# Kernel optimization log

Hardware: AMD Instinct MI355X
Metric: run time of the kernel (lower is better)

The kernel has to match this reference:

```python
import jax, jax.numpy as jnp
import numpy as np

DIM = 256; HEADS = 8; WS = 7; ALPHA = 0.5
HD = DIM // HEADS                      # head_dim = 32
GH = int(HEADS * ALPHA); LH = HEADS - GH   # 4 global / 4 local heads
GD = GH * HD; LD = LH * HD             # 128 / 128
HID = int(DIM * 4.0)                   # mlp hidden = 1024
SCALE = HD ** -0.5


def ln(x, g, b, eps=1e-5):
    m = jnp.mean(x, -1, keepdims=True)
    v = jnp.var(x, -1, keepdims=True)
    return (x - m) * jax.lax.rsqrt(v + eps) * g + b


def setup_inputs() -> dict:
    key = jax.random.key(0)
    ks = jax.random.split(key, 12)
    B, H, W = 4, 112, 112
    N = H * W
    def p(k, shape, s=0.02):
        return jax.random.normal(k, shape, jnp.float32) * s
    return {
        'x': jax.random.normal(ks[0], (B, N, DIM), jnp.float32),
        'x_reverse': jax.random.normal(ks[1], (B, N, DIM), jnp.float32),
        'g1': jnp.ones((DIM,), jnp.float32), 'b1': jnp.zeros((DIM,), jnp.float32),
        'g2': jnp.ones((DIM,), jnp.float32), 'b2': jnp.zeros((DIM,), jnp.float32),
        'Gq_w': p(ks[2], (DIM, GD)), 'Gq_b': jnp.zeros((GD,), jnp.float32),
        'Gkv_w': p(ks[3], (DIM, 2 * GD)), 'Gkv_b': jnp.zeros((2 * GD,), jnp.float32),
        'Gp_w': p(ks[4], (GD, GD)), 'Gp_b': jnp.zeros((GD,), jnp.float32),
        'Lq_w': p(ks[5], (DIM, LD)), 'Lq_b': jnp.zeros((LD,), jnp.float32),
        'Lkv_w': p(ks[6], (DIM, 2 * LD)), 'Lkv_b': jnp.zeros((2 * LD,), jnp.float32),
        'Lp_w': p(ks[7], (LD, LD)), 'Lp_b': jnp.zeros((LD,), jnp.float32),
        'fc1_w': p(ks[8], (DIM, HID)), 'fc1_b': jnp.zeros((HID,), jnp.float32),
        'dw_w': p(ks[9], (HID, 1, 3, 3), 0.05), 'dw_b': jnp.zeros((HID,), jnp.float32),
        'fc2_w': p(ks[10], (HID, DIM)), 'fc2_b': jnp.zeros((DIM,), jnp.float32),
        'H': 112, 'W': 112,
    }


def reference(x, x_reverse, g1, b1, g2, b2,
              Gq_w, Gq_b, Gkv_w, Gkv_b, Gp_w, Gp_b,
              Lq_w, Lq_b, Lkv_w, Lkv_b, Lp_w, Lp_b,
              fc1_w, fc1_b, dw_w, dw_b, fc2_w, fc2_b, H, W):
    B, N, C = x.shape
    assert H % WS == 0 and W % WS == 0  # shapes chosen so no padding branch
    xn = ln(x, g1, b1).reshape(B, H, W, C)
    xrn = ln(x_reverse, g1, b1).reshape(B, H, W, C)

    # ---- Global attention: queries from every pixel, kv from avg-pooled (ws x ws) grid
    q = (xn.reshape(B, N, C) @ Gq_w + Gq_b).reshape(B, N, GH, HD)
    pooled = xrn.reshape(B, H // WS, WS, W // WS, WS, C).mean(axis=(2, 4)).reshape(B, -1, C)
    kv = (pooled @ Gkv_w + Gkv_b).reshape(B, -1, 2, GH, HD)
    k, v = kv[:, :, 0], kv[:, :, 1]
    a = jax.nn.softmax(jnp.einsum('bnhd,bmhd->bhnm', q, k) * SCALE, axis=-1)
    g_out = jnp.einsum('bhnm,bmhd->bnhd', a, v).reshape(B, H, W, GD) @ Gp_w + Gp_b

    # ---- Local windowed attention (ws x ws non-overlapping windows)
    hg, wg = H // WS, W // WS
    TG, T = hg * wg, WS * WS
    def windows(t):
        return t.reshape(B, hg, WS, wg, WS, C).transpose(0, 1, 3, 2, 4, 5).reshape(B, TG, T, C)
    xw, xrw = windows(xn), windows(xrn)
    ql = (xw @ Lq_w + Lq_b).reshape(B, TG, T, LH, HD)
    kvl = (xrw @ Lkv_w + Lkv_b).reshape(B, TG, T, 2, LH, HD)
    kl, vl = kvl[:, :, :, 0], kvl[:, :, :, 1]
    al = jax.nn.softmax(jnp.einsum('bgqhd,bgkhd->bghqk', ql, kl) * SCALE, axis=-1)
    lo = jnp.einsum('bghqk,bgkhd->bgqhd', al, vl).reshape(B, hg, wg, WS, WS, LD)
    lo = lo.transpose(0, 1, 3, 2, 4, 5).reshape(B, H, W, LD) @ Lp_w + Lp_b

    x = x + jnp.concatenate([g_out, lo], axis=-1).reshape(B, N, C)

    # ---- DWMlp: fc1 -> depthwise 3x3 conv -> GELU -> fc2
    h = ln(x, g2, b2) @ fc1_w + fc1_b
    himg = h.reshape(B, H, W, HID).transpose(0, 3, 1, 2)
    himg = jax.lax.conv_general_dilated(
        himg, dw_w, (1, 1), 'SAME', feature_group_count=HID,
        dimension_numbers=('NCHW', 'OIHW', 'NCHW')) + dw_b[None, :, None, None]
    h = jax.nn.gelu(himg.reshape(B, HID, N).transpose(0, 2, 1), approximate=False)
    return x + (h @ fc2_w + fc2_b)
```

## Files before the change

kernel.cpp:

```cpp
#include <hip/hip_runtime.h>
#include <hip/hip_bf16.h>
#include <math.h>

typedef __hip_bfloat16 bf16;
typedef __attribute__((ext_vector_type(8))) short bf16x8;
typedef __attribute__((ext_vector_type(4))) float f32x4;

static constexpr int B_  = 4;
static constexpr int Hh  = 112, Ww = 112;
static constexpr int Nn  = Hh * Ww;
static constexpr int Cc  = 256;
static constexpr int M_  = B_ * Nn;
static constexpr int GH_ = 4;
static constexpr int GD_ = 128;
static constexpr int LD_ = 128;
static constexpr int HID_ = 1024;
static constexpr int TG_ = 256;
static constexpr int T__ = 49;
static constexpr float SCALE_ = 0.17677669529663687f;

__device__ __forceinline__ float toF(const bf16 v)  { return __bfloat162float(v); }
__device__ __forceinline__ float toF(const float v) { return v; }
__device__ __forceinline__ void st_out(float* p, float v) { *p = v; }
__device__ __forceinline__ void st_out(bf16* p, float v)  { *p = __float2bfloat16(v); }

__device__ __forceinline__ void gload_lds16(const bf16* g, bf16* l) {
  using gvoid = const __attribute__((address_space(1))) void;
  using lvoid = __attribute__((address_space(3))) void;
  __builtin_amdgcn_global_load_lds((gvoid*)g, (lvoid*)l, 16, 0, 0);
}

__device__ __forceinline__ int win_row_map(int r) {
  int b  = r / Nn;
  int rr = r - b * Nn;
  int g  = rr / T__;
  int t  = rr - g * T__;
  int gh = g >> 4, gw = g & 15;
  int i  = t / 7,  j  = t - i * 7;
  int n  = (gh * 7 + i) * Ww + gw * 7 + j;
  return b * Nn + n;
}

__global__ void guard_fill_kernel(float* out) {
  out[threadIdx.x + blockIdx.x * 256] = 1.0e6f;
}

__global__ __launch_bounds__(256) void convert_all_kernel(
    const float* __restrict__ s0, const float* __restrict__ s1,
    const float* __restrict__ s2, const float* __restrict__ s3,
    const float* __restrict__ s4, const float* __restrict__ s5,
    const float* __restrict__ s6, const float* __restrict__ s7,
    bf16* __restrict__ wt) {
  int idx = blockIdx.x * 256 + threadIdx.x;
  const float* W; int K, N, base;
  if      (idx < 32768)  { W = s0; K = 256;  N = 128;  base = 0; }
  else if (idx < 98304)  { W = s1; K = 256;  N = 256;  base = 32768; }
  else if (idx < 114688) { W = s2; K = 128;  N = 128;  base = 98304; }
  else if (idx < 147456) { W = s3; K = 256;  N = 128;  base = 114688; }
  else if (idx < 212992) { W = s4; K = 256;  N = 256;  base = 147456; }
  else if (idx < 229376) { W = s5; K = 128;  N = 128;  base = 212992; }
  else if (idx < 491520) { W = s6; K = 256;  N = 1024; base = 229376; }
  else                   { W = s7; K = 1024; N = 256;  base = 491520; }
  int loc = idx - base;
  int n = loc / K, k = loc - n * K;
  wt[idx] = __float2bfloat16(W[(size_t)k * N + n]);
}

__global__ __launch_bounds__(256) void ln_dual_kernel(const float* __restrict__ x,
                                                      const float* __restrict__ xr,
                                                      const float* __restrict__ g,
                                                      const float* __restrict__ bta,
                                                      bf16* __restrict__ xn,
                                                      bf16* __restrict__ xrn) {
  const int tid = threadIdx.x;
  const int row = blockIdx.x * 4 + (tid >> 6);
  const int lane = tid & 63;
  const int c0 = lane * 4;
  const float* src = blockIdx.y ? xr : x;
  bf16* dst = blockIdx.y ? xrn : xn;
  float4 v = *(const float4*)(src + (size_t)row * Cc + c0);
  float s  = v.x + v.y + v.z + v.w;
  float ss = v.x * v.x + v.y * v.y + v.z * v.z + v.w * v.w;
  #pragma unroll
  for (int off = 1; off < 64; off <<= 1) {
    s  += __shfl_xor(s, off);
    ss += __shfl_xor(ss, off);
  }
  float mean = s * (1.0f / Cc);
  float var  = ss * (1.0f / Cc) - mean * mean;
  float r = rsqrtf(var + 1e-5f);
  float4 gv = *(const float4*)(g + c0);
  float4 bv = *(const float4*)(bta + c0);
  bf16 o[4];
  o[0] = __float2bfloat16((v.x - mean) * r * gv.x + bv.x);
  o[1] = __float2bfloat16((v.y - mean) * r * gv.y + bv.y);
  o[2] = __float2bfloat16((v.z - mean) * r * gv.z + bv.z);
  o[3] = __float2bfloat16((v.w - mean) * r * gv.w + bv.w);
  *(uint2*)(dst + (size_t)row * Cc + c0) = *(uint2*)o;
}

__global__ __launch_bounds__(64) void pool_kernel(const bf16* __restrict__ xrn,
                                                  bf16* __restrict__ pooled) {
  const int lane = threadIdx.x;
  const int c0 = lane * 4;
  const int g  = blockIdx.x;
  const int b  = blockIdx.y;
  const int gh = g >> 4, gw = g & 15;
  float acc[4] = {};
  union U4 { uint2 u; bf16 e[4]; };
  #pragma unroll
  for (int i = 0; i < 7; i++)
    for (int j = 0; j < 7; j++) {
      int n = (gh * 7 + i) * Ww + gw * 7 + j;
      U4 r4;
      r4.u = *(const uint2*)(xrn + ((size_t)b * Nn + n) * Cc + c0);
      #pragma unroll
      for (int u = 0; u < 4; u++) acc[u] += toF(r4.e[u]);
    }
  bf16 o[4];
  #pragma unroll
  for (int u = 0; u < 4; u++) o[u] = __float2bfloat16(acc[u] * (1.0f / 49.0f));
  *(uint2*)(pooled + ((size_t)b * TG_ + g) * Cc + c0) = *(uint2*)o;
}

template <typename OutT, bool WIN_A, bool RES>
__global__ __launch_bounds__(256) void mfma_gemm_kernel(const bf16* __restrict__ A,
                                                        const bf16* __restrict__ Wt,
                                                        const float* __restrict__ bias,
                                                        const float* __restrict__ res,
                                                        OutT* __restrict__ out,
                                                        int M, int N, int K) {
  __shared__ __align__(16) bf16 As[128 * 32];
  __shared__ __align__(16) bf16 Bs[128 * 32];
  const int tid = threadIdx.x;
  const int bm = blockIdx.y * 128, bn = blockIdx.x * 128;
  const int lane = tid & 63, w = tid >> 6;
  const int wm = (w >> 1) * 64, wn = (w & 1) * 64;

  const int srow0 = w * 32 + (lane >> 2);
  const int srow1 = srow0 + 16;
  const int kq    = (lane & 3) * 8;
  const int ar0 = bm + srow0, ar1 = bm + srow1;
  const int as0 = WIN_A ? win_row_map(ar0) : ar0;
  const int as1 = WIN_A ? win_row_map(ar1) : ar1;
  const bf16* Ag0 = A  + (size_t)as0 * K + kq;
  const bf16* Ag1 = A  + (size_t)as1 * K + kq;
  const bf16* Bg0 = Wt + (size_t)(bn + srow0) * K + kq;
  const bf16* Bg1 = Wt + (size_t)(bn + srow1) * K + kq;
  bf16* Al0 = &As[srow0 * 32 + kq];
  bf16* Al1 = &As[srow1 * 32 + kq];
  bf16* Bl0 = &Bs[srow0 * 32 + kq];
  bf16* Bl1 = &Bs[srow1 * 32 + kq];

  f32x4 acc[4][4];
  #pragma unroll
  for (int i = 0; i < 4; i++)
    #pragma unroll
    for (int j = 0; j < 4; j++) acc[i][j] = (f32x4){0.f, 0.f, 0.f, 0.f};

  const int r16  = lane & 15;
  const int koct = (lane >> 4) * 8;
  const int mrow = wm + r16;
  const int nrow = wn + r16;

  for (int k0 = 0; k0 < K; k0 += 32) {
    gload_lds16(Ag0 + k0, Al0);
    gload_lds16(Ag1 + k0, Al1);
    gload_lds16(Bg0 + k0, Bl0);
    gload_lds16(Bg1 + k0, Bl1);
    __syncthreads();
    bf16x8 af[4], bfr[4];
    #pragma unroll
    for (int i = 0; i < 4; i++) af[i]  = *(const bf16x8*)&As[(mrow + i * 16) * 32 + koct];
    #pragma unroll
    for (int j = 0; j < 4; j++) bfr[j] = *(const bf16x8*)&Bs[(nrow + j * 16) * 32 + koct];
    #pragma unroll
    for (int i = 0; i < 4; i++)
      #pragma unroll
      for (int j = 0; j < 4; j++)
        acc[i][j] = __builtin_amdgcn_mfma_f32_16x16x32_bf16(af[i], bfr[j], acc[i][j], 0, 0, 0);
    __syncthreads();
  }

  const int r0 = (lane >> 4) * 4;
  #pragma unroll
  for (int j = 0; j < 4; j++) {
    const int col = bn + wn + j * 16 + r16;
    const float bv = bias[col];
    #pragma unroll
    for (int i = 0; i < 4; i++) {
      const int rowb = bm + wm + i * 16 + r0;
      #pragma unroll
      for (int r = 0; r < 4; r++) {
        size_t ro = (size_t)(rowb + r) * N + col;
        float v = acc[i][j][r] + bv;
        if (RES) v += res[ro];
        st_out(out + ro, v);
      }
    }
  }
}

__global__ __launch_bounds__(256) void gattn_kernel(const bf16* __restrict__ q,
                                                    const bf16* __restrict__ kv,
                                                    bf16* __restrict__ out) {
  __shared__ __align__(16) bf16 Ks[256][40];
  __shared__ __align__(16) bf16 Vt[32][264];
  __shared__ __align__(16) bf16 Ps[4][32][40];
  const int tid = threadIdx.x;
  const int lane = tid & 63, w = tid >> 6;
  const int h = blockIdx.y, b = blockIdx.z;
  const int n0 = blockIdx.x * 128;
  const int r16 = lane & 15, oct = (lane >> 4) * 8;
  const bf16* kvb = kv + (size_t)b * TG_ * 256;

  {
    const int key = tid;
    const bf16* kp = kvb + (size_t)key * 256 + h * 32;
    *(uint4*)&Ks[key][0]  = *(const uint4*)(kp);
    *(uint4*)&Ks[key][8]  = *(const uint4*)(kp + 8);
    *(uint4*)&Ks[key][16] = *(const uint4*)(kp + 16);
    *(uint4*)&Ks[key][24] = *(const uint4*)(kp + 24);
    union { uint4 u[4]; bf16 e[32]; } vv;
    vv.u[0] = *(const uint4*)(kp + 128);
    vv.u[1] = *(const uint4*)(kp + 136);
    vv.u[2] = *(const uint4*)(kp + 144);
    vv.u[3] = *(const uint4*)(kp + 152);
    #pragma unroll
    for (int d = 0; d < 32; d++) Vt[d][key] = vv.e[d];
  }
  const size_t qbase0 = ((size_t)(b * Nn + n0 + w * 32 + r16)) * GD_ + h * 32 + oct;
  bf16x8 aq0 = *(const bf16x8*)(q + qbase0);
  bf16x8 aq1 = *(const bf16x8*)(q + qbase0 + (size_t)16 * GD_);
  __syncthreads();

  f32x4 rs0 = {0.f, 0.f, 0.f, 0.f}, rs1 = {0.f, 0.f, 0.f, 0.f};
  f32x4 ov[2][2];
  #pragma unroll
  for (int i = 0; i < 2; i++)
    #pragma unroll
    for (int dt = 0; dt < 2; dt++) ov[i][dt] = (f32x4){0.f, 0.f, 0.f, 0.f};

  for (int c0 = 0; c0 < 256; c0 += 32) {
    #pragma unroll
    for (int t = 0; t < 2; t++) {
      bf16x8 bk = *(const bf16x8*)&Ks[c0 + t * 16 + r16][oct];
      f32x4 s0 = __builtin_amdgcn_mfma_f32_16x16x32_bf16(aq0, bk, (f32x4){0.f,0.f,0.f,0.f}, 0, 0, 0);
      f32x4 s1 = __builtin_amdgcn_mfma_f32_16x16x32_bf16(aq1, bk, (f32x4){0.f,0.f,0.f,0.f}, 0, 0, 0);
      const int prow = (lane >> 4) * 4;
      const int pcol = t * 16 + r16;
      #pragma unroll
      for (int r = 0; r < 4; r++) {
        bf16 pb0 = __float2bfloat16(__expf(s0[r] * SCALE_));
        bf16 pb1 = __float2bfloat16(__expf(s1[r] * SCALE_));
        rs0[r] += toF(pb0);
        rs1[r] += toF(pb1);
        Ps[w][prow + r][pcol]      = pb0;
        Ps[w][16 + prow + r][pcol] = pb1;
      }
    }
    bf16x8 ap0 = *(const bf16x8*)&Ps[w][r16][oct];
    bf16x8 ap1 = *(const bf16x8*)&Ps[w][16 + r16][oct];
    #pragma unroll
    for (int dt = 0; dt < 2; dt++) {
      bf16x8 bv = *(const bf16x8*)&Vt[dt * 16 + r16][c0 + oct];
      ov[0][dt] = __builtin_amdgcn_mfma_f32_16x16x32_bf16(ap0, bv, ov[0][dt], 0, 0, 0);
      ov[1][dt] = __builtin_amdgcn_mfma_f32_16x16x32_bf16(ap1, bv, ov[1][dt], 0, 0, 0);
    }
  }
  #pragma unroll
  for (int off = 1; off < 16; off <<= 1) {
    #pragma unroll
    for (int r = 0; r < 4; r++) {
      rs0[r] += __shfl_xor(rs0[r], off);
      rs1[r] += __shfl_xor(rs1[r], off);
    }
  }
  const int orow0 = b * Nn + n0 + w * 32 + (lane >> 4) * 4;
  #pragma unroll
  for (int r = 0; r < 4; r++) {
    float inv0 = 1.0f / rs0[r];
    float inv1 = 1.0f / rs1[r];
    size_t ro0 = (size_t)(orow0 + r) * GD_ + h * 32;
    size_t ro1 = ro0 + (size_t)16 * GD_;
    #pragma unroll
    for (int dt = 0; dt < 2; dt++) {
      out[ro0 + dt * 16 + r16] = __float2bfloat16(ov[0][dt][r] * inv0);
      out[ro1 + dt * 16 + r16] = __float2bfloat16(ov[1][dt][r] * inv1);
    }
  }
}

__global__ __launch_bounds__(64) void lattn_kernel(const bf16* __restrict__ ql,
                                                   const bf16* __restrict__ kvl,
                                                   bf16* __restrict__ out) {
  __shared__ float ks[T__ * 32];
  __shared__ float vs[T__ * 32];
  const int tid = threadIdx.x;
  const int h = blockIdx.x, g = blockIdx.y, b = blockIdx.z;
  const size_t base = (((size_t)b * TG_ + g) * T__) * 256;
  for (int idx = tid; idx < T__ * 32; idx += 64) {
    int m = idx >> 5, d = idx & 31;
    ks[idx] = toF(kvl[base + (size_t)m * 256 + h * 32 + d]);
    vs[idx] = toF(kvl[base + (size_t)m * 256 + 128 + h * 32 + d]);
  }
  __syncthreads();
  if (tid < T__) {
    const size_t qoff = (((size_t)b * TG_ + g) * T__ + tid) * LD_ + h * 32;
    float qv[32];
    #pragma unroll
    for (int d = 0; d < 32; d++) qv[d] = toF(ql[qoff + d]) * SCALE_;
    float l = 0.f;
    float acc[32] = {};
    for (int m = 0; m < T__; m++) {
      const float* kr = ks + m * 32;
      const float* vr = vs + m * 32;
      float s = 0.f;
      #pragma unroll
      for (int d = 0; d < 32; d++) s = fmaf(qv[d], kr[d], s);
      float p = __expf(fminf(s, 60.f));
      l += p;
      #pragma unroll
      for (int d = 0; d < 32; d++) acc[d] = fmaf(p, vr[d], acc[d]);
    }
    const float rl = 1.0f / l;
    #pragma unroll
    for (int d = 0; d < 32; d++) out[qoff + d] = __float2bfloat16(acc[d] * rl);
  }
}

__global__ __launch_bounds__(256) void combine_ln_kernel(const float* __restrict__ x,
                                                         const bf16* __restrict__ gout,
                                                         const bf16* __restrict__ lo_w,
                                                         const float* __restrict__ g2,
                                                         const float* __restrict__ b2,
                                                         float* __restrict__ xres,
                                                         bf16* __restrict__ xn2) {
  const int tid = threadIdx.x;
  const int row = blockIdx.x * 4 + (tid >> 6);
  const int lane = tid & 63;
  const int c0 = lane * 4;
  int b = row / Nn, n = row - b * Nn;
  int y = n / Ww, xx = n - y * Ww;
  int gh = y / 7, i = y - gh * 7;
  int gw = xx / 7, j = xx - gw * 7;
  size_t wrow = ((size_t)b * TG_ + gh * 16 + gw) * T__ + i * 7 + j;
  union U4 { uint2 u; bf16 e[4]; } r4;
  if (lane < 32) r4.u = *(const uint2*)(gout + (size_t)row * GD_ + c0);
  else           r4.u = *(const uint2*)(lo_w + wrow * LD_ + (c0 - 128));
  float4 v = *(const float4*)(x + (size_t)row * Cc + c0);
  v.x += toF(r4.e[0]); v.y += toF(r4.e[1]); v.z += toF(r4.e[2]); v.w += toF(r4.e[3]);
  *(float4*)(xres + (size_t)row * Cc + c0) = v;
  float s  = v.x + v.y + v.z + v.w;
  float ss = v.x * v.x + v.y * v.y + v.z * v.z + v.w * v.w;
  #pragma unroll
  for (int off = 1; off < 64; off <<= 1) {
    s  += __shfl_xor(s, off);
    ss += __shfl_xor(ss, off);
  }
  float mean = s * (1.0f / Cc);
  float var  = ss * (1.0f / Cc) - mean * mean;
  float r = rsqrtf(var + 1e-5f);
  float4 gv = *(const float4*)(g2 + c0);
  float4 bv = *(const float4*)(b2 + c0);
  bf16 o[4];
  o[0] = __float2bfloat16((v.x - mean) * r * gv.x + bv.x);
  o[1] = __float2bfloat16((v.y - mean) * r * gv.y + bv.y);
  o[2] = __float2bfloat16((v.z - mean) * r * gv.z + bv.z);
  o[3] = __float2bfloat16((v.w - mean) * r * gv.w + bv.w);
  *(uint2*)(xn2 + (size_t)row * Cc + c0) = *(uint2*)o;
}

static constexpr int TW_ = 14;
__global__ __launch_bounds__(256) void dwconv_gelu_kernel(const bf16* __restrict__ h1,
                                                          const float* __restrict__ w,
                                                          const float* __restrict__ bias,
                                                          bf16* __restrict__ h2) {
  const int tid = threadIdx.x;
  const int c0 = tid * 4;
  const int img = blockIdx.z, y = blockIdx.y;
  const int xt = blockIdx.x * TW_;
  const size_t ibase = (size_t)img * Nn * HID_;

  float wreg[9][4], breg[4];
  #pragma unroll
  for (int u = 0; u < 4; u++) {
    breg[u] = bias[c0 + u];
    #pragma unroll
    for (int t = 0; t < 9; t++) wreg[t][u] = w[(c0 + u) * 9 + t];
  }

  const bf16* rowp[3];
  bool rok[3];
  #pragma unroll
  for (int r = 0; r < 3; r++) {
    int yy = y - 1 + r;
    rok[r] = (yy >= 0 && yy < Hh);
    rowp[r] = h1 + ibase + (size_t)(rok[r] ? yy : 0) * Ww * HID_ + c0;
  }

  float wa[3][4], wb[3][4], wc[3][4];
  union U4 { ushort2 u2[2]; bf16 e[4]; };
  auto loadcol = [&](int xcol, float v[3][4]) {
    if (xcol < 0 || xcol >= Ww) {
      #pragma unroll
      for (int r = 0; r < 3; r++)
        #pragma unroll
        for (int u = 0; u < 4; u++) v[r][u] = 0.f;
      return;
    }
    #pragma unroll
    for (int r = 0; r < 3; r++) {
      if (rok[r]) {
        U4 raw;
        *(uint2*)&raw = *(const uint2*)(rowp[r] + (size_t)xcol * HID_);
        #pragma unroll
        for (int u = 0; u < 4; u++) v[r][u] = toF(raw.e[u]);
      } else {
        #pragma unroll
        for (int u = 0; u < 4; u++) v[r][u] = 0.f;
      }
    }
  };
  loadcol(xt - 1, wa);
  loadcol(xt, wb);

  for (int xx = 0; xx < TW_; xx++) {
    const int x = xt + xx;
    loadcol(x + 1, wc);
    bf16 res[4];
    #pragma unroll
    for (int u = 0; u < 4; u++) {
      float a = breg[u];
      a = fmaf(wa[0][u], wreg[0][u], a);
      a = fmaf(wb[0][u], wreg[1][u], a);
      a = fmaf(wc[0][u], wreg[2][u], a);
      a = fmaf(wa[1][u], wreg[3][u], a);
      a = fmaf(wb[1][u], wreg[4][u], a);
      a = fmaf(wc[1][u], wreg[5][u], a);
      a = fmaf(wa[2][u], wreg[6][u], a);
      a = fmaf(wb[2][u], wreg[7][u], a);
      a = fmaf(wc[2][u], wreg[8][u], a);
      float gl = 0.5f * a * (1.0f + erff(a * 0.7071067811865475f));
      res[u] = __float2bfloat16(gl);
    }
    *(uint2*)(h2 + ibase + (size_t)(y * Ww + x) * HID_ + c0) = *(uint2*)res;
    #pragma unroll
    for (int r = 0; r < 3; r++)
      #pragma unroll
      for (int u = 0; u < 4; u++) { wa[r][u] = wb[r][u]; wb[r][u] = wc[r][u]; }
  }
}

extern "C" void kernel_launch(void* const* d_in, const int* in_sizes, int n_in,
                              void* d_out, int out_size, void* d_ws, size_t ws_size,
                              hipStream_t stream) {
  const float* x     = (const float*)d_in[0];
  const float* xrev  = (const float*)d_in[1];
  const float* g1    = (const float*)d_in[2];
  const float* b1    = (const float*)d_in[3];
  const float* g2    = (const float*)d_in[4];
  const float* b2    = (const float*)d_in[5];
  const float* Gq_w  = (const float*)d_in[6];
  const float* Gq_b  = (const float*)d_in[7];
  const float* Gkv_w = (const float*)d_in[8];
  const float* Gkv_b = (const float*)d_in[9];
  const float* Gp_w  = (const float*)d_in[10];
  const float* Gp_b  = (const float*)d_in[11];
  const float* Lq_w  = (const float*)d_in[12];
  const float* Lq_b  = (const float*)d_in[13];
  const float* Lkv_w = (const float*)d_in[14];
  const float* Lkv_b = (const float*)d_in[15];
  const float* Lp_w  = (const float*)d_in[16];
  const float* Lp_b  = (const float*)d_in[17];
  const float* fc1_w = (const float*)d_in[18];
  const float* fc1_b = (const float*)d_in[19];
  const float* dw_w  = (const float*)d_in[20];
  const float* dw_b  = (const float*)d_in[21];
  const float* fc2_w = (const float*)d_in[22];
  const float* fc2_b = (const float*)d_in[23];

  const size_t E_GQ = 256 * 128, E_GKV = 256 * 256, E_GP = 128 * 128;
  const size_t E_LQ = 256 * 128, E_LKV = 256 * 256, E_LP = 128 * 128;
  const size_t E_F1 = 256 * 1024, E_F2 = 1024 * 256;
  char* ws = (char*)d_ws;
  bf16* Gq_t  = (bf16*)ws;
  bf16* Gkv_t = Gq_t  + E_GQ;
  bf16* Gp_t  = Gkv_t + E_GKV;
  bf16* Lq_t  = Gp_t  + E_GP;
  bf16* Lkv_t = Lq_t  + E_LQ;
  bf16* Lp_t  = Lkv_t + E_LKV;
  bf16* f1_t  = Lp_t  + E_LP;
  bf16* f2_t  = f1_t  + E_F1;
  const size_t WT_ELEMS = E_GQ + E_GKV + E_GP + E_LQ + E_LKV + E_LP + E_F1 + E_F2;
  const size_t WT_BYTES = WT_ELEMS * 2;

  const size_t SZ_ROW2 = (size_t)M_ * Cc * 2;
  const size_t SZ_HALF = (size_t)M_ * 128 * 2;
  const size_t SZ_POOL = (size_t)B_ * TG_ * Cc * 2;
  const size_t SZ_KVG  = (size_t)B_ * TG_ * 256 * 2;
  const size_t SZ_H    = (size_t)(2 * Nn) * HID_ * 2;
  char* arena = ws + WT_BYTES;
  bf16* S1 = (bf16*)(arena);
  bf16* S2 = (bf16*)(arena + SZ_ROW2);
  bf16* S3 = (bf16*)(arena + 2 * SZ_ROW2);
  bf16* S4 = (bf16*)(arena + 2 * SZ_ROW2 + SZ_HALF);
  bf16* S5 = (bf16*)(arena + 2 * SZ_ROW2 + 2 * SZ_HALF);
  bf16* poolb = (bf16*)(arena + 2 * SZ_ROW2 + 3 * SZ_HALF);
  bf16* kvG   = (bf16*)(arena + 2 * SZ_ROW2 + 3 * SZ_HALF + SZ_POOL);
  const size_t ARENA_A = 2 * SZ_ROW2 + 3 * SZ_HALF + SZ_POOL + SZ_KVG;
  bf16* xn2 = S1;
  bf16* h1  = (bf16*)(arena + SZ_ROW2);
  bf16* h2  = (bf16*)(arena + SZ_ROW2 + SZ_H);
  const size_t ARENA_B = SZ_ROW2 + 2 * SZ_H;

  float* out  = (float*)d_out;
  float* xres = (float*)d_out;
  const size_t NEED = WT_BYTES + (ARENA_A > ARENA_B ? ARENA_A : ARENA_B);
  if (ws_size < NEED) {
    guard_fill_kernel<<<16, 256, 0, stream>>>(out);
    return;
  }

  bf16* xn = S1;  bf16* xrn = S2;  bf16* qbuf = S3;  bf16* gattn = S4;  bf16* gout = S5;
  bf16* kvl = S1; bf16* lo_w = S2; bf16* qlb  = S3;  bf16* lattn = S4;

  convert_all_kernel<<<2944, 256, 0, stream>>>(Gq_w, Gkv_w, Gp_w, Lq_w, Lkv_w, Lp_w,
                                               fc1_w, fc2_w, (bf16*)ws);
  ln_dual_kernel<<<dim3(M_ / 4, 2), 256, 0, stream>>>(x, xrev, g1, b1, xn, xrn);
  pool_kernel<<<dim3(TG_, B_), 64, 0, stream>>>(xrn, poolb);
  mfma_gemm_kernel<bf16, false, false><<<dim3(1, M_ / 128), 256, 0, stream>>>(
      xn, Gq_t, Gq_b, nullptr, qbuf, M_, 128, 256);
  mfma_gemm_kernel<bf16, false, false><<<dim3(2, 8), 256, 0, stream>>>(
      poolb, Gkv_t, Gkv_b, nullptr, kvG, 1024, 256, 256);
  gattn_kernel<<<dim3(Nn / 128, GH_, B_), 256, 0, stream>>>(qbuf, kvG, gattn);
  mfma_gemm_kernel<bf16, false, false><<<dim3(1, M_ / 128), 256, 0, stream>>>(
      gattn, Gp_t, Gp_b, nullptr, gout, M_, 128, 128);
  mfma_gemm_kernel<bf16, true, false><<<dim3(1, M_ / 128), 256, 0, stream>>>(
      xn, Lq_t, Lq_b, nullptr, qlb, M_, 128, 256);
  mfma_gemm_kernel<bf16, true, false><<<dim3(2, M_ / 128), 256, 0, stream>>>(
      xrn, Lkv_t, Lkv_b, nullptr, kvl, M_, 256, 256);
  lattn_kernel<<<dim3(4, TG_, B_), 64, 0, stream>>>(qlb, kvl, lattn);
  mfma_gemm_kernel<bf16, false, false><<<dim3(1, M_ / 128), 256, 0, stream>>>(
      lattn, Lp_t, Lp_b, nullptr, lo_w, M_, 128, 128);
  combine_ln_kernel<<<M_ / 4, 256, 0, stream>>>(x, gout, lo_w, g2, b2, xres, xn2);
  for (int half = 0; half < 2; half++) {
    const size_t r0 = (size_t)half * 2 * Nn;
    mfma_gemm_kernel<bf16, false, false><<<dim3(8, (2 * Nn) / 128), 256, 0, stream>>>(
        xn2 + r0 * Cc, f1_t, fc1_b, nullptr, h1, 2 * Nn, 1024, 256);
    dwconv_gelu_kernel<<<dim3(Ww / TW_, Hh, 2), 256, 0, stream>>>(h1, dw_w, dw_b, h2);
    mfma_gemm_kernel<float, false, true><<<dim3(2, (2 * Nn) / 128), 256, 0, stream>>>(
        h2, f2_t, fc2_b, xres + r0 * Cc, out + r0 * Cc, 2 * Nn, 256, 1024);
  }
}
```

Before: 556.2 us.

## Rewrite local window attention with MFMA, one block per window

The local attention kernel changes from one thread per query doing scalar fp32 dot products over shared-memory K/V to a 256-thread block per window, with each wave handling one head. QK^T and PV now use bf16 16x16x32 MFMA instructions. K is staged row-major, V is staged transposed, and the bf16 probabilities are written to shared memory. The 49-token window is padded to 64 with masking and zeroed V columns. This removes the scalar FMA bottleneck and the idle lanes of the old 64-thread blocks. In exchange, P is quantized to bf16, and the score clamp before exp is dropped, so there is no overflow guard.

```diff
diff --git a/kernel.cpp b/kernel.cpp
--- a/kernel.cpp
+++ b/kernel.cpp
@@ -291,41 +291,106 @@
   }
 }
 
-__global__ __launch_bounds__(64) void lattn_kernel(const bf16* __restrict__ ql,
-                                                   const bf16* __restrict__ kvl,
-                                                   bf16* __restrict__ out) {
-  __shared__ float ks[T__ * 32];
-  __shared__ float vs[T__ * 32];
+__global__ __launch_bounds__(256) void lattn_kernel(const bf16* __restrict__ ql,
+                                                    const bf16* __restrict__ kvl,
+                                                    bf16* __restrict__ out) {
+  __shared__ __align__(16) bf16 Ks[4][64][40];
+  __shared__ __align__(16) bf16 Vt[4][32][72];
+  __shared__ __align__(16) bf16 Ps[4][64][72];
   const int tid = threadIdx.x;
-  const int h = blockIdx.x, g = blockIdx.y, b = blockIdx.z;
-  const size_t base = (((size_t)b * TG_ + g) * T__) * 256;
-  for (int idx = tid; idx < T__ * 32; idx += 64) {
-    int m = idx >> 5, d = idx & 31;
-    ks[idx] = toF(kvl[base + (size_t)m * 256 + h * 32 + d]);
-    vs[idx] = toF(kvl[base + (size_t)m * 256 + 128 + h * 32 + d]);
+  const int lane = tid & 63, w = tid >> 6;
+  const int g = blockIdx.x, b = blockIdx.y;
+  const int r16 = lane & 15, oct = (lane >> 4) * 8;
+  const size_t wbase = ((size_t)b * TG_ + g) * T__;
+
+  for (int u = tid; u < T__ * 32; u += 256) {
+    int m = u >> 5, c8 = u & 31;
+    union { uint4 q4; bf16 e[8]; } ch;
+    ch.q4 = *(const uint4*)(kvl + (wbase + m) * 256 + c8 * 8);
+    if (c8 < 16) {
+      int h = c8 >> 2, d0 = (c8 & 3) * 8;
+      *(uint4*)&Ks[h][m][d0] = ch.q4;
+    } else {
+      int cv = c8 - 16;
+      int h = cv >> 2, d0 = (cv & 3) * 8;
+      #pragma unroll
+      for (int e = 0; e < 8; e++) Vt[h][d0 + e][m] = ch.e[e];
+    }
+  }
+  for (int z = tid; z < 4 * 32 * 15; z += 256) {
+    int h = z / 480, rem = z - h * 480;
+    int d = rem / 15, key = 49 + (rem - d * 15);
+    Vt[h][d][key] = __float2bfloat16(0.f);
+  }
+  bf16x8 aq[4];
+  #pragma unroll
+  for (int i = 0; i < 4; i++) {
+    int qr = 16 * i + r16;
+    if (qr > 48) qr = 48;
+    aq[i] = *(const bf16x8*)(ql + (wbase + qr) * LD_ + w * 32 + oct);
   }
   __syncthreads();
-  if (tid < T__) {
-    const size_t qoff = (((size_t)b * TG_ + g) * T__ + tid) * LD_ + h * 32;
-    float qv[32];
-    #pragma unroll
-    for (int d = 0; d < 32; d++) qv[d] = toF(ql[qoff + d]) * SCALE_;
-    float l = 0.f;
-    float acc[32] = {};
-    for (int m = 0; m < T__; m++) {
-      const float* kr = ks + m * 32;
-      const float* vr = vs + m * 32;
-      float s = 0.f;
-      #pragma unroll
-      for (int d = 0; d < 32; d++) s = fmaf(qv[d], kr[d], s);
-      float p = __expf(fminf(s, 60.f));
-      l += p;
-      #pragma unroll
-      for (int d = 0; d < 32; d++) acc[d] = fmaf(p, vr[d], acc[d]);
-    }
-    const float rl = 1.0f / l;
-    #pragma unroll
-    for (int d = 0; d < 32; d++) out[qoff + d] = __float2bfloat16(acc[d] * rl);
+
+  f32x4 s[4][4];
+  #pragma unroll
+  for (int j = 0; j < 4; j++) {
+    bf16x8 bk = *(const bf16x8*)&Ks[w][16 * j + r16][oct];
+    #pragma unroll
+    for (int i = 0; i < 4; i++)
+      s[i][j] = __builtin_amdgcn_mfma_f32_16x16x32_bf16(aq[i], bk, (f32x4){0.f,0.f,0.f,0.f}, 0, 0, 0);
+  }
+
+  const int prow = (lane >> 4) * 4;
+  float rs[4][4];
+  #pragma unroll
+  for (int i = 0; i < 4; i++) {
+    #pragma unroll
+    for (int r = 0; r < 4; r++) {
+      float acc = 0.f;
+      #pragma unroll
+      for (int j = 0; j < 4; j++) {
+        float p = __expf(s[i][j][r] * SCALE_);
+        if (j == 3 && r16 != 0) p = 0.f;
+        bf16 pb = __float2bfloat16(p);
+        Ps[w][16 * i + prow + r][16 * j + r16] = pb;
+        acc += toF(pb);
+      }
+      #pragma unroll
+      for (int off = 1; off < 16; off <<= 1) acc += __shfl_xor(acc, off);
+      rs[i][r] = acc;
+    }
+  }
+
+  f32x4 ov[4][2];
+  #pragma unroll
+  for (int i = 0; i < 4; i++) {
+    ov[i][0] = (f32x4){0.f, 0.f, 0.f, 0.f};
+    ov[i][1] = (f32x4){0.f, 0.f, 0.f, 0.f};
+  }
+  #pragma unroll
+  for (int kc = 0; kc < 2; kc++) {
+    bf16x8 bv0 = *(const bf16x8*)&Vt[w][r16][kc * 32 + oct];
+    bf16x8 bv1 = *(const bf16x8*)&Vt[w][16 + r16][kc * 32 + oct];
+    #pragma unroll
+    for (int i = 0; i < 4; i++) {
+      bf16x8 ap = *(const bf16x8*)&Ps[w][16 * i + r16][kc * 32 + oct];
+      ov[i][0] = __builtin_amdgcn_mfma_f32_16x16x32_bf16(ap, bv0, ov[i][0], 0, 0, 0);
+      ov[i][1] = __builtin_amdgcn_mfma_f32_16x16x32_bf16(ap, bv1, ov[i][1], 0, 0, 0);
+    }
+  }
+
+  #pragma unroll
+  for (int i = 0; i < 4; i++) {
+    #pragma unroll
+    for (int r = 0; r < 4; r++) {
+      int qr = 16 * i + prow + r;
+      if (qr < T__) {
+        float inv = 1.0f / rs[i][r];
+        size_t o = (wbase + qr) * LD_ + w * 32;
+        out[o + r16]      = __float2bfloat16(ov[i][0][r] * inv);
+        out[o + 16 + r16] = __float2bfloat16(ov[i][1][r] * inv);
+      }
+    }
   }
 }
 
@@ -540,7 +605,7 @@
       xn, Lq_t, Lq_b, nullptr, qlb, M_, 128, 256);
   mfma_gemm_kernel<bf16, true, false><<<dim3(2, M_ / 128), 256, 0, stream>>>(
       xrn, Lkv_t, Lkv_b, nullptr, kvl, M_, 256, 256);
-  lattn_kernel<<<dim3(4, TG_, B_), 64, 0, stream>>>(qlb, kvl, lattn);
+  lattn_kernel<<<dim3(TG_, B_), 256, 0, stream>>>(qlb, kvl, lattn);
   mfma_gemm_kernel<bf16, false, false><<<dim3(1, M_ / 128), 256, 0, stream>>>(
       lattn, Lp_t, Lp_b, nullptr, lo_w, M_, 128, 128);
   combine_ln_kernel<<<M_ / 4, 256, 0, stream>>>(x, gout, lo_w, g2, b2, xres, xn2);
```

Measured after the change: 542.8 us. 1.02x faster.
